# Kernel optimization log

Hardware: AMD Instinct MI355X
Metric: run time of the kernel (lower is better)

The kernel has to match this reference:

```python
import jax, jax.numpy as jnp
import numpy as np

INPUT_DIM = 28
OUTPUT_DIM = 21
LAYER_SIZE = 64
NUM_HIDDEN = 10  # number of 64x64 hidden layers after the input layer


def setup_inputs() -> dict:
    key = jax.random.key(0)
    ks = jax.random.split(key, 7)
    x = jax.random.normal(ks[0], (1048576, INPUT_DIM), dtype=jnp.float32)
    # PyTorch nn.Linear default init: U(-1/sqrt(fan_in), 1/sqrt(fan_in)); plain uniform is fine for a baseline.
    s_in = 1.0 / np.sqrt(INPUT_DIM)
    s_h = 1.0 / np.sqrt(LAYER_SIZE)
    W_in = jax.random.uniform(ks[1], (INPUT_DIM, LAYER_SIZE), jnp.float32, -s_in, s_in)
    b_in = jax.random.uniform(ks[2], (LAYER_SIZE,), jnp.float32, -s_in, s_in)
    W_hid = jax.random.uniform(ks[3], (NUM_HIDDEN, LAYER_SIZE, LAYER_SIZE), jnp.float32, -s_h, s_h)
    b_hid = jax.random.uniform(ks[4], (NUM_HIDDEN, LAYER_SIZE), jnp.float32, -s_h, s_h)
    W_out = jax.random.uniform(ks[5], (LAYER_SIZE, OUTPUT_DIM), jnp.float32, -s_h, s_h)
    b_out = jax.random.uniform(ks[6], (OUTPUT_DIM,), jnp.float32, -s_h, s_h)
    return {"x": x, "W_in": W_in, "b_in": b_in, "W_hid": W_hid, "b_hid": b_hid,
            "W_out": W_out, "b_out": b_out}


def reference(x, W_in, b_in, W_hid, b_hid, W_out, b_out):
    h = jax.nn.relu(x @ W_in + b_in)  # [B, 64]
    def step(h, wb):
        W, b = wb
        return jax.nn.relu(h @ W + b), None
    h, _ = jax.lax.scan(step, h, (W_hid, b_hid))
    return jax.nn.sigmoid(h @ W_out + b_out)  # [B, 21]
```

## Files before the change

### kernel.cpp

```cpp
#include <hip/hip_runtime.h>

#define DEV __device__ __forceinline__

typedef _Float16 half8 __attribute__((ext_vector_type(8)));
typedef _Float16 half2v __attribute__((ext_vector_type(2)));
typedef float f32x16 __attribute__((ext_vector_type(16)));
typedef int int4v __attribute__((ext_vector_type(4)));

DEV f32x16 mfma16(half8 a, half8 b, f32x16 c) {
    return __builtin_amdgcn_mfma_f32_32x32x16_f16(a, b, c, 0, 0, 0);
}
DEV half8 h8(int4v v) { return __builtin_bit_cast(half8, v); }
DEV half8 ldh8(const _Float16* p) { return *(const half8*)p; }
DEV int pkrtz(float a, float b) {
    auto t = __builtin_amdgcn_cvt_pkrtz(a, b);
    return __builtin_bit_cast(int, t);
}
DEV int relupk(float a, float b) {
    int p = pkrtz(a, b);
    half2v h = __builtin_bit_cast(half2v, p);
    half2v z = {(_Float16)0.f, (_Float16)0.f};
    h = __builtin_elementwise_max(h, z);
    return __builtin_bit_cast(int, h);
}
DEV void plswap(int& a, int& b) {
    asm("v_permlane32_swap_b32 %0, %1" : "+v"(a), "+v"(b));
}

DEV f32x16 zero16() {
    f32x16 z = {0.f,0.f,0.f,0.f,0.f,0.f,0.f,0.f,0.f,0.f,0.f,0.f,0.f,0.f,0.f,0.f};
    return z;
}

struct Frags { int4v c[4]; };

DEV void repack(const f32x16& C0, const f32x16& C1, Frags& B) {
    int P0[8], P1[8];
#pragma unroll
    for (int q = 0; q < 8; ++q) {
        P0[q] = relupk(C0[2*q], C0[2*q+1]);
        P1[q] = relupk(C1[2*q], C1[2*q+1]);
    }
#pragma unroll
    for (int kk = 0; kk < 4; ++kk) {
        const int* Pm = (kk < 2) ? P0 : P1;
        int idx = 4 * (kk & 1);
        int a0 = Pm[idx + 0], b0 = Pm[idx + 2];
        int a1 = Pm[idx + 1], b1 = Pm[idx + 3];
        plswap(a0, b0);
        plswap(a1, b1);
        int4v nb; nb[0] = a0; nb[1] = a1; nb[2] = b0; nb[3] = b1;
        B.c[kk] = nb;
    }
}

DEV void loadA5(const _Float16* base, int lam, half8* A0, half8* A1) {
    const _Float16* p0 = base + lam * 8;
    const _Float16* p1 = base + 2560 + lam * 8;
#pragma unroll
    for (int kk = 0; kk < 5; ++kk) {
        A0[kk] = ldh8(p0 + kk * 512);
        A1[kk] = ldh8(p1 + kk * 512);
    }
}

DEV void mfma_hid_t(const half8* A0, const half8* A1, int4v ones, const Frags& Bx,
                    f32x16& C0, f32x16& C1) {
    C0 = mfma16(A0[4], h8(ones), zero16());
    C1 = mfma16(A1[4], h8(ones), zero16());
#pragma unroll
    for (int kk = 0; kk < 4; ++kk) {
        half8 b = h8(Bx.c[kk]);
        C0 = mfma16(A0[kk], b, C0);
        C1 = mfma16(A1[kk], b, C1);
    }
}

DEV void mfma_in_t(const half8* I, const Frags& Bx, f32x16& C0, f32x16& C1) {
    C0 = mfma16(I[0], h8(Bx.c[0]), zero16());
    C1 = mfma16(I[2], h8(Bx.c[0]), zero16());
    C0 = mfma16(I[1], h8(Bx.c[1]), C0);
    C1 = mfma16(I[3], h8(Bx.c[1]), C1);
}

DEV void mfma_out_t(const half8* Ao, int4v ones, const Frags& Bx, f32x16& C) {
    C = mfma16(Ao[4], h8(ones), zero16());
#pragma unroll
    for (int kk = 0; kk < 4; ++kk) C = mfma16(Ao[kk], h8(Bx.c[kk]), C);
}

DEV void store_out(const f32x16& C, int h, float* __restrict__ out, int row) {
    float* o = out + row * 21;
#pragma unroll
    for (int r = 0; r < 16; ++r) {
        int f = (r & 3) + 8 * (r >> 2) + 4 * h;
        if (f < 21) o[f] = __builtin_amdgcn_rcpf(1.f + __expf(-C[r]));
    }
}

DEV void load_x(const float* __restrict__ x, int row, int h, Frags& B) {
    const float* xr = x + row * 28;
    float4 fa = *(const float4*)(xr + 8 * h);
    float4 fb = *(const float4*)(xr + 8 * h + 4);
    float4 fc = *(const float4*)(xr + 16 + 8 * h);
    float4 fd = (h == 0) ? *(const float4*)(xr + 20) : make_float4(1.f, 0.f, 0.f, 0.f);
    int4v c0, c1;
    c0[0] = pkrtz(fa.x, fa.y); c0[1] = pkrtz(fa.z, fa.w);
    c0[2] = pkrtz(fb.x, fb.y); c0[3] = pkrtz(fb.z, fb.w);
    c1[0] = pkrtz(fc.x, fc.y); c1[1] = pkrtz(fc.z, fc.w);
    c1[2] = pkrtz(fd.x, fd.y); c1[3] = pkrtz(fd.z, fd.w);
    B.c[0] = c0; B.c[1] = c1;
}

#define NT 512

__global__ __attribute__((amdgpu_flat_work_group_size(NT, NT), amdgpu_waves_per_eu(2, 2)))
void mlp_fused(
    const float* __restrict__ x, const float* __restrict__ W_in, const float* __restrict__ b_in,
    const float* __restrict__ W_hid, const float* __restrict__ b_hid,
    const float* __restrict__ W_out, const float* __restrict__ b_out,
    float* __restrict__ out) {
    __shared__ __align__(16) _Float16 wH[51200];
    __shared__ __align__(16) _Float16 wI[2048];
    __shared__ __align__(16) _Float16 wO[2560];

    const int tid = threadIdx.x;

    for (int i = tid; i < 10240; i += NT) {
        int l = i >> 10, rem = i & 1023, m = rem >> 9, off = rem & 511;
        wH[l * 5120 + m * 2560 + 2048 + off] = (_Float16)0.f;
    }
    for (int i = tid; i < 2048; i += NT) wI[i] = (_Float16)0.f;
    for (int i = tid; i < 2560; i += NT) wO[i] = (_Float16)0.f;
    __syncthreads();

    for (int i = tid; i < 40960; i += NT) {
        int o = i & 63, kin = (i >> 6) & 63, l = i >> 12;
        int m = o >> 5, kk = kin >> 4, hh = (kin >> 3) & 1, e = kin & 7;
        int lam = hh * 32 + (o & 31);
        wH[l * 5120 + m * 2560 + kk * 512 + lam * 8 + e] = (_Float16)W_hid[i];
    }
    for (int i = tid; i < 640; i += NT) {
        int l = i >> 6, f = i & 63, m = f >> 5, r = f & 31;
        wH[l * 5120 + m * 2560 + 2048 + r * 8] = (_Float16)b_hid[i];
    }
    for (int i = tid; i < 1792; i += NT) {
        int o = i & 63, kin = i >> 6;
        int m = o >> 5, kk = kin >> 4, hh = (kin >> 3) & 1, e = kin & 7;
        int lam = hh * 32 + (o & 31);
        wI[m * 1024 + kk * 512 + lam * 8 + e] = (_Float16)W_in[i];
    }
    for (int i = tid; i < 64; i += NT) {
        int m = i >> 5;
        wI[m * 1024 + 512 + (32 + (i & 31)) * 8 + 4] = (_Float16)b_in[i];
    }
    for (int i = tid; i < 1344; i += NT) {
        int o = i % 21, kin = i / 21;
        int kk = kin >> 4, hh = (kin >> 3) & 1, e = kin & 7;
        int lam = hh * 32 + o;
        wO[kk * 512 + lam * 8 + e] = (_Float16)W_out[i];
    }
    for (int i = tid; i < 21; i += NT)
        wO[4 * 512 + i * 8] = (_Float16)b_out[i];
    __syncthreads();

    const int w = tid >> 6, lam = tid & 63;
    const int col = lam & 31, h = lam >> 5;
    int4v ones; ones[0] = (h == 0) ? 0x3C00 : 0; ones[1] = 0; ones[2] = 0; ones[3] = 0;

    half8 I[4], Ao[5];
    {
        const _Float16* p0 = wI + lam * 8;
        const _Float16* p1 = wI + 1024 + lam * 8;
        I[0] = ldh8(p0);       I[1] = ldh8(p0 + 512);
        I[2] = ldh8(p1);       I[3] = ldh8(p1 + 512);
        const _Float16* po = wO + lam * 8;
#pragma unroll
        for (int kk = 0; kk < 5; ++kk) Ao[kk] = ldh8(po + kk * 512);
    }

    const int tbase = blockIdx.x * 128;
#pragma unroll 1
    for (int j = 0; j < 8; ++j) {
        int tA = tbase + w * 16 + 2 * j;
        int rowA = tA * 32 + col, rowB = rowA + 32;
        Frags BA, BB;
        load_x(x, rowA, h, BA);
        load_x(x, rowB, h, BB);

        half8 Fa0[5], Fa1[5], Fb0[5], Fb1[5];
        f32x16 CA0, CA1, CB0, CB1;

        mfma_in_t(I, BA, CA0, CA1);
        loadA5(wH, lam, Fa0, Fa1);
        mfma_in_t(I, BB, CB0, CB1);
        repack(CA0, CA1, BA);

#pragma unroll
        for (int l2 = 0; l2 < 5; ++l2) {
            const _Float16* b0 = wH + (2 * l2) * 5120;
            mfma_hid_t(Fa0, Fa1, ones, BA, CA0, CA1);
            loadA5(b0 + 5120, lam, Fb0, Fb1);
            repack(CB0, CB1, BB);
            mfma_hid_t(Fa0, Fa1, ones, BB, CB0, CB1);
            repack(CA0, CA1, BA);
            mfma_hid_t(Fb0, Fb1, ones, BA, CA0, CA1);
            if (l2 < 4) loadA5(b0 + 10240, lam, Fa0, Fa1);
            repack(CB0, CB1, BB);
            mfma_hid_t(Fb0, Fb1, ones, BB, CB0, CB1);
            repack(CA0, CA1, BA);
        }

        f32x16 CoA, CoB;
        mfma_out_t(Ao, ones, BA, CoA);
        repack(CB0, CB1, BB);
        mfma_out_t(Ao, ones, BB, CoB);
        store_out(CoA, h, out, rowA);
        store_out(CoB, h, out, rowB);
    }
}

extern "C" void kernel_launch(void* const* d_in, const int* in_sizes, int n_in,
                              void* d_out, int out_size, void* d_ws, size_t ws_size,
                              hipStream_t stream) {
    const float* x     = (const float*)d_in[0];
    const float* W_in  = (const float*)d_in[1];
    const float* b_in  = (const float*)d_in[2];
    const float* W_hid = (const float*)d_in[3];
    const float* b_hid = (const float*)d_in[4];
    const float* W_out = (const float*)d_in[5];
    const float* b_out = (const float*)d_in[6];
    float* out = (float*)d_out;
    mlp_fused<<<dim3(256), dim3(NT), 0, stream>>>(x, W_in, b_in, W_hid, b_hid, W_out, b_out, out);
}
```

Baseline: 100.7 us.

## Fold hidden biases into fp16 repack instead of extra bias MFMA

Drops the fifth MFMA per hidden layer, which added the bias through a ones-vector times a bias row. The bias is instead added in packed fp16 during the ReLU repack, using per-lane bias values preloaded from a small LDS table. The output bias is used as the initial MFMA accumulator. This cuts MFMA work by about a fifth and shrinks the weight LDS footprint, but the bias is now added in fp16 after rounding, a small precision change, and the input weights are reloaded from LDS on every loop iteration.

```diff
diff --git a/kernel.cpp b/kernel.cpp
--- a/kernel.cpp
+++ b/kernel.cpp
@@ -16,31 +16,27 @@
     auto t = __builtin_amdgcn_cvt_pkrtz(a, b);
     return __builtin_bit_cast(int, t);
 }
-DEV int relupk(float a, float b) {
+DEV int pk_bias_relu(float a, float b, int biaspk) {
     int p = pkrtz(a, b);
-    half2v h = __builtin_bit_cast(half2v, p);
+    half2v s = __builtin_bit_cast(half2v, p) + __builtin_bit_cast(half2v, biaspk);
     half2v z = {(_Float16)0.f, (_Float16)0.f};
-    h = __builtin_elementwise_max(h, z);
-    return __builtin_bit_cast(int, h);
+    s = __builtin_elementwise_max(s, z);
+    return __builtin_bit_cast(int, s);
+}
+DEV int pk_relu(float a, float b) {
+    int p = pkrtz(a, b);
+    half2v s = __builtin_bit_cast(half2v, p);
+    half2v z = {(_Float16)0.f, (_Float16)0.f};
+    s = __builtin_elementwise_max(s, z);
+    return __builtin_bit_cast(int, s);
 }
 DEV void plswap(int& a, int& b) {
     asm("v_permlane32_swap_b32 %0, %1" : "+v"(a), "+v"(b));
 }
 
-DEV f32x16 zero16() {
-    f32x16 z = {0.f,0.f,0.f,0.f,0.f,0.f,0.f,0.f,0.f,0.f,0.f,0.f,0.f,0.f,0.f,0.f};
-    return z;
-}
-
 struct Frags { int4v c[4]; };
 
-DEV void repack(const f32x16& C0, const f32x16& C1, Frags& B) {
-    int P0[8], P1[8];
-#pragma unroll
-    for (int q = 0; q < 8; ++q) {
-        P0[q] = relupk(C0[2*q], C0[2*q+1]);
-        P1[q] = relupk(C1[2*q], C1[2*q+1]);
-    }
+DEV void swap_pack(const int* P0, const int* P1, Frags& B) {
 #pragma unroll
     for (int kk = 0; kk < 4; ++kk) {
         const int* Pm = (kk < 2) ? P0 : P1;
@@ -54,39 +50,65 @@
     }
 }
 
-DEV void loadA5(const _Float16* base, int lam, half8* A0, half8* A1) {
+DEV void repack_b(const f32x16& C0, const f32x16& C1, const int4v* Bq, Frags& B) {
+    int P0[8], P1[8];
+#pragma unroll
+    for (int q = 0; q < 8; ++q) {
+        int b0 = (q < 4) ? Bq[0][q & 3] : Bq[1][q & 3];
+        int b1 = (q < 4) ? Bq[2][q & 3] : Bq[3][q & 3];
+        P0[q] = pk_bias_relu(C0[2*q], C0[2*q+1], b0);
+        P1[q] = pk_bias_relu(C1[2*q], C1[2*q+1], b1);
+    }
+    swap_pack(P0, P1, B);
+}
+DEV void repack_nb(const f32x16& C0, const f32x16& C1, Frags& B) {
+    int P0[8], P1[8];
+#pragma unroll
+    for (int q = 0; q < 8; ++q) {
+        P0[q] = pk_relu(C0[2*q], C0[2*q+1]);
+        P1[q] = pk_relu(C1[2*q], C1[2*q+1]);
+    }
+    swap_pack(P0, P1, B);
+}
+
+DEV void loadA4(const _Float16* base, int lam, half8* A0, half8* A1) {
     const _Float16* p0 = base + lam * 8;
-    const _Float16* p1 = base + 2560 + lam * 8;
-#pragma unroll
-    for (int kk = 0; kk < 5; ++kk) {
+    const _Float16* p1 = base + 2048 + lam * 8;
+#pragma unroll
+    for (int kk = 0; kk < 4; ++kk) {
         A0[kk] = ldh8(p0 + kk * 512);
         A1[kk] = ldh8(p1 + kk * 512);
     }
 }
-
-DEV void mfma_hid_t(const half8* A0, const half8* A1, int4v ones, const Frags& Bx,
-                    f32x16& C0, f32x16& C1) {
-    C0 = mfma16(A0[4], h8(ones), zero16());
-    C1 = mfma16(A1[4], h8(ones), zero16());
-#pragma unroll
-    for (int kk = 0; kk < 4; ++kk) {
+DEV void loadBias(const int* biasPk, int l, int h, int4v* Bq) {
+    const int* p = biasPk + l * 32 + h * 8;
+    Bq[0] = *(const int4v*)(p);
+    Bq[1] = *(const int4v*)(p + 4);
+    Bq[2] = *(const int4v*)(p + 16);
+    Bq[3] = *(const int4v*)(p + 20);
+}
+
+DEV void mfma_hid8(const half8* A0, const half8* A1, const Frags& Bx, const f32x16& Z,
+                   f32x16& C0, f32x16& C1) {
+    C0 = mfma16(A0[0], h8(Bx.c[0]), Z);
+    C1 = mfma16(A1[0], h8(Bx.c[0]), Z);
+#pragma unroll
+    for (int kk = 1; kk < 4; ++kk) {
         half8 b = h8(Bx.c[kk]);
         C0 = mfma16(A0[kk], b, C0);
         C1 = mfma16(A1[kk], b, C1);
     }
 }
-
-DEV void mfma_in_t(const half8* I, const Frags& Bx, f32x16& C0, f32x16& C1) {
-    C0 = mfma16(I[0], h8(Bx.c[0]), zero16());
-    C1 = mfma16(I[2], h8(Bx.c[0]), zero16());
+DEV void mfma_in4(const half8* I, const Frags& Bx, const f32x16& Z, f32x16& C0, f32x16& C1) {
+    C0 = mfma16(I[0], h8(Bx.c[0]), Z);
+    C1 = mfma16(I[2], h8(Bx.c[0]), Z);
     C0 = mfma16(I[1], h8(Bx.c[1]), C0);
     C1 = mfma16(I[3], h8(Bx.c[1]), C1);
 }
-
-DEV void mfma_out_t(const half8* Ao, int4v ones, const Frags& Bx, f32x16& C) {
-    C = mfma16(Ao[4], h8(ones), zero16());
-#pragma unroll
-    for (int kk = 0; kk < 4; ++kk) C = mfma16(Ao[kk], h8(Bx.c[kk]), C);
+DEV void mfma_out4(const half8* Ao, const Frags& Bx, const f32x16& bo, f32x16& C) {
+    C = mfma16(Ao[0], h8(Bx.c[0]), bo);
+#pragma unroll
+    for (int kk = 1; kk < 4; ++kk) C = mfma16(Ao[kk], h8(Bx.c[kk]), C);
 }
 
 DEV void store_out(const f32x16& C, int h, float* __restrict__ out, int row) {
@@ -120,29 +142,29 @@
     const float* __restrict__ W_hid, const float* __restrict__ b_hid,
     const float* __restrict__ W_out, const float* __restrict__ b_out,
     float* __restrict__ out) {
-    __shared__ __align__(16) _Float16 wH[51200];
+    __shared__ __align__(16) _Float16 wH[40960];
     __shared__ __align__(16) _Float16 wI[2048];
-    __shared__ __align__(16) _Float16 wO[2560];
+    __shared__ __align__(16) _Float16 wO[2048];
+    __shared__ __align__(16) _Float16 biasPkH[640];
+    __shared__ __align__(16) float biasOut[32];
 
     const int tid = threadIdx.x;
 
-    for (int i = tid; i < 10240; i += NT) {
-        int l = i >> 10, rem = i & 1023, m = rem >> 9, off = rem & 511;
-        wH[l * 5120 + m * 2560 + 2048 + off] = (_Float16)0.f;
-    }
-    for (int i = tid; i < 2048; i += NT) wI[i] = (_Float16)0.f;
-    for (int i = tid; i < 2560; i += NT) wO[i] = (_Float16)0.f;
+    for (int i = tid; i < 2048; i += NT) { wI[i] = (_Float16)0.f; wO[i] = (_Float16)0.f; }
     __syncthreads();
 
     for (int i = tid; i < 40960; i += NT) {
         int o = i & 63, kin = (i >> 6) & 63, l = i >> 12;
         int m = o >> 5, kk = kin >> 4, hh = (kin >> 3) & 1, e = kin & 7;
         int lam = hh * 32 + (o & 31);
-        wH[l * 5120 + m * 2560 + kk * 512 + lam * 8 + e] = (_Float16)W_hid[i];
+        wH[l * 4096 + m * 2048 + kk * 512 + lam * 8 + e] = (_Float16)W_hid[i];
     }
     for (int i = tid; i < 640; i += NT) {
-        int l = i >> 6, f = i & 63, m = f >> 5, r = f & 31;
-        wH[l * 5120 + m * 2560 + 2048 + r * 8] = (_Float16)b_hid[i];
+        int u = i >> 1, j = i & 1;
+        int l = u >> 5, rem = u & 31, m = rem >> 4, hh = (rem >> 3) & 1, q = rem & 7;
+        int rr = 2 * q + j;
+        int f = (rr & 3) + 8 * (rr >> 2) + 4 * hh + 32 * m;
+        biasPkH[u * 2 + j] = (_Float16)b_hid[l * 64 + f];
     }
     for (int i = tid; i < 1792; i += NT) {
         int o = i & 63, kin = i >> 6;
@@ -160,24 +182,37 @@
         int lam = hh * 32 + o;
         wO[kk * 512 + lam * 8 + e] = (_Float16)W_out[i];
     }
-    for (int i = tid; i < 21; i += NT)
-        wO[4 * 512 + i * 8] = (_Float16)b_out[i];
+    for (int i = tid; i < 32; i += NT) {
+        int hh = i >> 4, r = i & 15;
+        int f = (r & 3) + 8 * (r >> 2) + 4 * hh;
+        biasOut[i] = (f < 21) ? b_out[f] : 0.f;
+    }
     __syncthreads();
 
     const int w = tid >> 6, lam = tid & 63;
     const int col = lam & 31, h = lam >> 5;
-    int4v ones; ones[0] = (h == 0) ? 0x3C00 : 0; ones[1] = 0; ones[2] = 0; ones[3] = 0;
-
-    half8 I[4], Ao[5];
+    const int* biasPk = (const int*)biasPkH;
+
+    half8 Ao[4];
     {
-        const _Float16* p0 = wI + lam * 8;
-        const _Float16* p1 = wI + 1024 + lam * 8;
-        I[0] = ldh8(p0);       I[1] = ldh8(p0 + 512);
-        I[2] = ldh8(p1);       I[3] = ldh8(p1 + 512);
         const _Float16* po = wO + lam * 8;
 #pragma unroll
-        for (int kk = 0; kk < 5; ++kk) Ao[kk] = ldh8(po + kk * 512);
-    }
+        for (int kk = 0; kk < 4; ++kk) Ao[kk] = ldh8(po + kk * 512);
+    }
+    f32x16 bo;
+    {
+        float4 b0 = *(const float4*)(biasOut + h * 16);
+        float4 b1 = *(const float4*)(biasOut + h * 16 + 4);
+        float4 b2 = *(const float4*)(biasOut + h * 16 + 8);
+        float4 b3 = *(const float4*)(biasOut + h * 16 + 12);
+        bo[0]=b0.x; bo[1]=b0.y; bo[2]=b0.z; bo[3]=b0.w;
+        bo[4]=b1.x; bo[5]=b1.y; bo[6]=b1.z; bo[7]=b1.w;
+        bo[8]=b2.x; bo[9]=b2.y; bo[10]=b2.z; bo[11]=b2.w;
+        bo[12]=b3.x; bo[13]=b3.y; bo[14]=b3.z; bo[15]=b3.w;
+    }
+    f32x16 Z;
+#pragma unroll
+    for (int r = 0; r < 16; ++r) Z[r] = 0.f;
 
     const int tbase = blockIdx.x * 128;
 #pragma unroll 1
@@ -187,34 +222,46 @@
         Frags BA, BB;
         load_x(x, rowA, h, BA);
         load_x(x, rowB, h, BB);
-
-        half8 Fa0[5], Fa1[5], Fb0[5], Fb1[5];
+        half8 I[4];
+        {
+            const _Float16* p0 = wI + lam * 8;
+            const _Float16* p1 = wI + 1024 + lam * 8;
+            I[0] = ldh8(p0); I[1] = ldh8(p0 + 512);
+            I[2] = ldh8(p1); I[3] = ldh8(p1 + 512);
+        }
+
+        half8 Fa0[4], Fa1[4], Fb0[4], Fb1[4];
+        int4v Ba[4], Bb[4];
         f32x16 CA0, CA1, CB0, CB1;
 
-        mfma_in_t(I, BA, CA0, CA1);
-        loadA5(wH, lam, Fa0, Fa1);
-        mfma_in_t(I, BB, CB0, CB1);
-        repack(CA0, CA1, BA);
+        mfma_in4(I, BA, Z, CA0, CA1);
+        loadA4(wH, lam, Fa0, Fa1);
+        mfma_in4(I, BB, Z, CB0, CB1);
+        loadBias(biasPk, 0, h, Ba);
+        repack_nb(CA0, CA1, BA);
 
 #pragma unroll
         for (int l2 = 0; l2 < 5; ++l2) {
-            const _Float16* b0 = wH + (2 * l2) * 5120;
-            mfma_hid_t(Fa0, Fa1, ones, BA, CA0, CA1);
-            loadA5(b0 + 5120, lam, Fb0, Fb1);
-            repack(CB0, CB1, BB);
-            mfma_hid_t(Fa0, Fa1, ones, BB, CB0, CB1);
-            repack(CA0, CA1, BA);
-            mfma_hid_t(Fb0, Fb1, ones, BA, CA0, CA1);
-            if (l2 < 4) loadA5(b0 + 10240, lam, Fa0, Fa1);
-            repack(CB0, CB1, BB);
-            mfma_hid_t(Fb0, Fb1, ones, BB, CB0, CB1);
-            repack(CA0, CA1, BA);
+            const _Float16* base = wH + (2 * l2) * 4096;
+            mfma_hid8(Fa0, Fa1, BA, Z, CA0, CA1);
+            loadA4(base + 4096, lam, Fb0, Fb1);
+            if (l2 == 0) repack_nb(CB0, CB1, BB);
+            else         repack_b(CB0, CB1, Bb, BB);
+            mfma_hid8(Fa0, Fa1, BB, Z, CB0, CB1);
+            loadBias(biasPk, 2 * l2 + 1, h, Bb);
+            repack_b(CA0, CA1, Ba, BA);
+            mfma_hid8(Fb0, Fb1, BA, Z, CA0, CA1);
+            if (l2 < 4) loadA4(base + 8192, lam, Fa0, Fa1);
+            repack_b(CB0, CB1, Ba, BB);
+            mfma_hid8(Fb0, Fb1, BB, Z, CB0, CB1);
+            if (l2 < 4) loadBias(biasPk, 2 * l2 + 2, h, Ba);
+            repack_b(CA0, CA1, Bb, BA);
         }
 
         f32x16 CoA, CoB;
-        mfma_out_t(Ao, ones, BA, CoA);
-        repack(CB0, CB1, BB);
-        mfma_out_t(Ao, ones, BB, CoB);
+        mfma_out4(Ao, BA, bo, CoA);
+        repack_b(CB0, CB1, Bb, BB);
+        mfma_out4(Ao, BB, bo, CoB);
         store_out(CoA, h, out, rowA);
         store_out(CoB, h, out, rowB);
     }
```

Measured after the change: 104.1 us. 3.4% more time.
